# Optimization experiments

Hardware: AMD Instinct MI355X
Metric: run time of the kernel (lower is better)

Reference implementation:

```python
import jax, jax.numpy as jnp
import numpy as np

N_NODES = 4096
N_EDGES = 65536
BS = 16
LEAKY_SLOPE = 0.01
BN_EPS = 1e-5


def _init(key, shape, scale=0.02):
    return (jax.random.normal(key, shape, dtype=jnp.float32) * scale)


def setup_inputs() -> dict:
    key = jax.random.key(0)
    ks = jax.random.split(key, 20)
    x_in = jax.random.normal(ks[0], (N_NODES, 8500), dtype=jnp.float32)
    edge_index = jax.random.randint(ks[1], (2, N_EDGES), 0, N_NODES, dtype=jnp.int64)
    return {
        "x_in": x_in,
        "edge_index": edge_index,
        # SAGEConv params: Wl (neighbor lin, with bias), Wr (root lin, no bias)
        "W1l": _init(ks[2], (320, 8500)), "b1": jnp.zeros((320,), jnp.float32), "W1r": _init(ks[3], (320, 8500)),
        "W2l": _init(ks[4], (180, 320)),  "b2": jnp.zeros((180,), jnp.float32), "W2r": _init(ks[5], (180, 320)),
        "W3l": _init(ks[6], (90, 180)),   "b3": jnp.zeros((90,), jnp.float32),  "W3r": _init(ks[7], (90, 180)),
        "W4l": _init(ks[8], (50, 90)),    "b4": jnp.zeros((50,), jnp.float32),  "W4r": _init(ks[9], (50, 90)),
        "Wf1": _init(ks[10], (32, 50)),   "bf1": jnp.zeros((32,), jnp.float32),
        "Wf2": _init(ks[11], (16, 32)),   "bf2": jnp.zeros((16,), jnp.float32),
        "Wf3": _init(ks[12], (1, 16)),    "bf3": jnp.zeros((1,), jnp.float32),
    }


def _sage(x, src, dst, Wl, bl, Wr):
    # PyG SAGEConv: out = lin_l(mean_{j in N(i)} x_j) + lin_r(x_i)
    agg = jax.ops.segment_sum(x[src], dst, num_segments=N_NODES)          # [N, F]
    deg = jax.ops.segment_sum(jnp.ones_like(dst, dtype=x.dtype), dst, num_segments=N_NODES)
    mean = agg / jnp.maximum(deg, 1.0)[:, None]
    return mean @ Wl.T + bl + x @ Wr.T


def _leaky(x):
    return jnp.where(x >= 0, x, LEAKY_SLOPE * x)


def _bn(x):
    # F.batch_norm(x, None, None, training=True): per-feature, biased var, no affine
    m = jnp.mean(x, axis=0)
    v = jnp.mean((x - m) ** 2, axis=0)
    return (x - m) / jnp.sqrt(v + BN_EPS)


def reference(x_in, edge_index,
              W1l, b1, W1r, W2l, b2, W2r, W3l, b3, W3r, W4l, b4, W4r,
              Wf1, bf1, Wf2, bf2, Wf3, bf3):
    src, dst = edge_index[0], edge_index[1]
    x = _bn(_leaky(_sage(x_in, src, dst, W1l, b1, W1r)))
    x = _bn(_leaky(_sage(x, src, dst, W2l, b2, W2r)))
    x = _bn(_leaky(_sage(x, src, dst, W3l, b3, W3r)))
    x = _bn(_leaky(_sage(x, src, dst, W4l, b4, W4r)))
    # get_batch: label i -> floor(i / (N/BS)); global_add_pool == segment sum
    x = x.reshape(BS, N_NODES // BS, -1).sum(axis=1)                      # [BS, 50]
    x = x @ Wf1.T + bf1
    x = x @ Wf2.T + bf2
    x = x @ Wf3.T + bf3
    return x
```

## Files before the change

kernel.cpp:

```cpp
#include <hip/hip_runtime.h>
#include <stdint.h>

#define NN 4096
#define NE 65536
#define LEAKY 0.01f
#define BN_EPS 1e-5f
#define DSTRIDE 96

typedef float f32x4 __attribute__((ext_vector_type(4)));
typedef __bf16 bf16x8 __attribute__((ext_vector_type(8)));
typedef unsigned short u16x8 __attribute__((ext_vector_type(8)));

static __device__ __forceinline__ unsigned short f2bf(float v) {
  unsigned int u = __float_as_uint(v);
  u += 0x7fff + ((u >> 16) & 1);
  return (unsigned short)(u >> 16);
}

typedef __attribute__((address_space(1))) void gvoid;
typedef __attribute__((address_space(3))) void lvoid;

static __device__ __forceinline__ void async16(const void* g, void* l) {
  __builtin_amdgcn_global_load_lds((gvoid*)(uintptr_t)g,
                                   (lvoid*)(uint32_t)(uintptr_t)l, 16, 0, 0);
}


static __device__ __forceinline__ void pack_w_seg(int lblk, const float* __restrict__ Wl,
                                                  const float* __restrict__ Wr,
                                                  unsigned short* __restrict__ dst,
                                                  int Fout, int Fin, int Kp, int Np) {
  int nb = Kp >> 3;
  int idx = lblk * 256 + threadIdx.x;
  if (idx >= Np * nb) return;
  int row = idx / nb, kb = idx - row * nb;
  int g = kb >> 3, b = kb & 7;
  int dkb = (g << 3) | ((b + row) & 7);
  const float* src = nullptr;
  if (row < Fout)          src = Wl + (size_t)row * Fin;
  else if (row < 2 * Fout) src = Wr + (size_t)(row - Fout) * Fin;
  u16x8 st;
#pragma unroll
  for (int o = 0; o < 8; ++o) {
    int k = kb * 8 + o;
    float v = (src && k < Fin) ? src[k] : 0.f;
    st[o] = f2bf(v);
  }
  *(u16x8*)&dst[(size_t)row * Kp + dkb * 8] = st;
}

#define ADJ_BLK    256
#define PW1_BLK   2660
#define PW2_BLK     60
#define PW3_BLK     24
#define PW4_BLK      8
#define SETUP_BLK (ADJ_BLK + PW1_BLK + PW2_BLK + PW3_BLK + PW4_BLK)

__global__ __launch_bounds__(256) void setup_all(
    const int* __restrict__ esrc, const int* __restrict__ edst,
    const float* __restrict__ W1l, const float* __restrict__ W1r,
    const float* __restrict__ W2l, const float* __restrict__ W2r,
    const float* __restrict__ W3l, const float* __restrict__ W3r,
    const float* __restrict__ W4l, const float* __restrict__ W4r,
    unsigned short* __restrict__ wb1, unsigned short* __restrict__ wb2,
    unsigned short* __restrict__ wb3, unsigned short* __restrict__ wb4,
    int* __restrict__ deg, int* __restrict__ eix) {
  int blk = blockIdx.x;
  if (blk < ADJ_BLK) {
    int e = blk * 256 + threadIdx.x;
    int d = edst[e];
    int pos = atomicAdd(&deg[d], 1);
    if (pos < DSTRIDE) eix[(size_t)d * DSTRIDE + pos] = esrc[e];
  } else if (blk < ADJ_BLK + PW1_BLK) {
    pack_w_seg(blk - ADJ_BLK, W1l, W1r, wb1, 320, 8500, 8512, 640);
  } else if (blk < ADJ_BLK + PW1_BLK + PW2_BLK) {
    pack_w_seg(blk - ADJ_BLK - PW1_BLK, W2l, W2r, wb2, 180, 320, 320, 384);
  } else if (blk < ADJ_BLK + PW1_BLK + PW2_BLK + PW3_BLK) {
    pack_w_seg(blk - ADJ_BLK - PW1_BLK - PW2_BLK, W3l, W3r, wb3, 90, 180, 192, 256);
  } else {
    pack_w_seg(blk - ADJ_BLK - PW1_BLK - PW2_BLK - PW3_BLK, W4l, W4r, wb4,
               50, 90, 128, 128);
  }
}

__global__ __launch_bounds__(256) void gemm_f32a(const float* __restrict__ X,
                                                 const unsigned short* __restrict__ B,
                                                 float* __restrict__ C, int N, int M) {
  const int K = 8512, KS = 133, FIN = 8500;
  __shared__ unsigned short smem[3 * 128 * 64];
  unsigned short* As = smem;

  const int t = threadIdx.x;
  const int bm = blockIdx.x, bn = blockIdx.y;
  const int lane = t & 63;
  const int wave = t >> 6;
  const int wm = (wave & 1) * 64, wn = (wave >> 1) * 64;
  const int l16 = lane & 15, quad = lane >> 4;

  const int gz = (int)gridDim.z, z = (int)blockIdx.z;
  const int per = KS / gz, rem = KS % gz;
  const int k0 = z * per + (z < rem ? z : rem);
  const int k1 = k0 + per + (z < rem ? 1 : 0);

  f32x4 acc[4][4];
#pragma unroll
  for (int i = 0; i < 4; ++i)
#pragma unroll
    for (int j = 0; j < 4; ++j) acc[i][j] = (f32x4){0.f, 0.f, 0.f, 0.f};

  const int srow = t >> 3;
  const int bblk = t & 7;
  const int scol = bblk * 8;
  const float* Xb = X + (size_t)(bm * 128) * FIN;
  const unsigned short* Bbase = B + (size_t)(bn * 128) * K + scol;

  float va[4][8];
  auto loadA = [&](int kt) {
    int gc = kt * 64 + scol;
#pragma unroll
    for (int p = 0; p < 4; ++p) {
      const float* ap = Xb + (size_t)(p * 32 + srow) * FIN + gc;
      if (gc + 8 <= FIN) {
        f32x4 a = *(const f32x4*)ap;
        f32x4 b2 = *(const f32x4*)(ap + 4);
#pragma unroll
        for (int o = 0; o < 4; ++o) { va[p][o] = a[o]; va[p][o + 4] = b2[o]; }
      } else {
#pragma unroll
        for (int o = 0; o < 8; ++o) va[p][o] = (gc + o < FIN) ? ap[o] : 0.f;
      }
    }
  };
  auto writeA = [&]() {
#pragma unroll
    for (int p = 0; p < 4; ++p) {
      int row = p * 32 + srow;
      int rot = ((bblk + row) & 7) * 8;
      bf16x8 bv;
#pragma unroll
      for (int o = 0; o < 8; ++o) bv[o] = (__bf16)va[p][o];
      *(bf16x8*)&As[row * 64 + rot] = bv;
    }
  };
  auto stageB = [&](int kt, int bb) {
    unsigned short* Bd = smem + 128 * 64 + bb * 128 * 64;
#pragma unroll
    for (int p = 0; p < 4; ++p) {
      int row = p * 32 + srow;
      async16(Bbase + (size_t)row * K + kt * 64, &Bd[row * 64 + scol]);
    }
  };

  loadA(k0);
  stageB(k0, 0);
  writeA();
  __syncthreads();

  int bb = 0;
  for (int kt = k0; kt < k1; ++kt) {
    bool more = (kt + 1 < k1);
    if (more) {
      loadA(kt + 1);
      stageB(kt + 1, bb ^ 1);
    }
    const unsigned short* Bs = smem + 128 * 64 + bb * 128 * 64;
#pragma unroll
    for (int kh = 0; kh < 2; ++kh) {
      const int s8 = ((kh * 4 + quad + l16) & 7) * 8;
      bf16x8 af[4], bfr[4];
#pragma unroll
      for (int i = 0; i < 4; ++i)
        af[i] = *(const bf16x8*)&As[(wm + i * 16 + l16) * 64 + s8];
#pragma unroll
      for (int j = 0; j < 4; ++j)
        bfr[j] = *(const bf16x8*)&Bs[(wn + j * 16 + l16) * 64 + s8];
#pragma unroll
      for (int i = 0; i < 4; ++i)
#pragma unroll
        for (int j = 0; j < 4; ++j)
          acc[i][j] = __builtin_amdgcn_mfma_f32_16x16x32_bf16(af[i], bfr[j], acc[i][j], 0, 0, 0);
    }
    __syncthreads();
    if (more) {
      writeA();
      __syncthreads();
      bb ^= 1;
    }
  }

  float* Cb = C + (size_t)blockIdx.z * M * N;
#pragma unroll
  for (int i = 0; i < 4; ++i) {
    int rbase = bm * 128 + wm + i * 16 + quad * 4;
#pragma unroll
    for (int j = 0; j < 4; ++j) {
      int col = bn * 128 + wn + j * 16 + l16;
      float* cp = Cb + (size_t)rbase * N + col;
#pragma unroll
      for (int r = 0; r < 4; ++r) cp[(size_t)r * N] = acc[i][j][r];
    }
  }
}

__global__ __launch_bounds__(256) void gemm_bt(const unsigned short* __restrict__ A,
                                               const unsigned short* __restrict__ B,
                                               float* __restrict__ C, int N, int K,
                                               int M) {
  __shared__ unsigned short smem[2 * 128 * 64];
  unsigned short* As = smem;
  unsigned short* Bs = smem + 128 * 64;

  const int t = threadIdx.x;
  const int bm = blockIdx.x, bn = blockIdx.y;
  const int lane = t & 63;
  const int wave = t >> 6;
  const int wm = (wave & 1) * 64, wn = (wave >> 1) * 64;
  const int l16 = lane & 15, quad = lane >> 4;

  const int ksteps = K >> 6;

  f32x4 acc[4][4];
#pragma unroll
  for (int i = 0; i < 4; ++i)
#pragma unroll
    for (int j = 0; j < 4; ++j) acc[i][j] = (f32x4){0.f, 0.f, 0.f, 0.f};

  const int srow = t >> 3;
  const int scol = (t & 7) * 8;
  const unsigned short* Abase = A + (size_t)(bm * 128) * K + scol;
  const unsigned short* Bbase = B + (size_t)(bn * 128) * K + scol;

  for (int kt = 0; kt < ksteps; ++kt) {
    const unsigned short* Ag = Abase + kt * 64;
    const unsigned short* Bg = Bbase + kt * 64;
#pragma unroll
    for (int p = 0; p < 4; ++p) {
      int row = p * 32 + srow;
      async16(Ag + (size_t)row * K, &As[row * 64 + scol]);
    }
#pragma unroll
    for (int p = 0; p < 4; ++p) {
      int row = p * 32 + srow;
      async16(Bg + (size_t)row * K, &Bs[row * 64 + scol]);
    }
    __syncthreads();
#pragma unroll
    for (int kh = 0; kh < 2; ++kh) {
      const int s8 = ((kh * 4 + quad + l16) & 7) * 8;
      bf16x8 af[4], bfr[4];
#pragma unroll
      for (int i = 0; i < 4; ++i)
        af[i] = *(const bf16x8*)&As[(wm + i * 16 + l16) * 64 + s8];
#pragma unroll
      for (int j = 0; j < 4; ++j)
        bfr[j] = *(const bf16x8*)&Bs[(wn + j * 16 + l16) * 64 + s8];
#pragma unroll
      for (int i = 0; i < 4; ++i)
#pragma unroll
        for (int j = 0; j < 4; ++j)
          acc[i][j] = __builtin_amdgcn_mfma_f32_16x16x32_bf16(af[i], bfr[j], acc[i][j], 0, 0, 0);
    }
    __syncthreads();
  }

#pragma unroll
  for (int i = 0; i < 4; ++i) {
    int rbase = bm * 128 + wm + i * 16 + quad * 4;
#pragma unroll
    for (int j = 0; j < 4; ++j) {
      int col = bn * 128 + wn + j * 16 + l16;
      float* cp = C + (size_t)rbase * N + col;
#pragma unroll
      for (int r = 0; r < 4; ++r) cp[(size_t)r * N] = acc[i][j][r];
    }
  }
}

__global__ void reduceN(float* __restrict__ y, int nz) {
  int idx = blockIdx.x * 256 + threadIdx.x;
  f32x4* p = (f32x4*)y;
  const int S = NN * 640 / 4;
  f32x4 v = p[idx];
  for (int sl = 1; sl < nz; ++sl) v += p[idx + (size_t)sl * S];
  p[idx] = v;
}

__global__ __launch_bounds__(256) void sage_agg(
    const float* __restrict__ y, const int* __restrict__ deg,
    const int* __restrict__ eix, const float* __restrict__ bias,
    float* __restrict__ z, int F, int ldy) {
  int i = blockIdx.x;
  int tx = threadIdx.x, ty = threadIdx.y;
  __shared__ int se[DSTRIDE];
  __shared__ float red[3][64][4];
  int d = deg[i]; if (d > DSTRIDE) d = DSTRIDE;
  {
    int lt = ty * 64 + tx;
    if (lt < d) se[lt] = eix[(size_t)i * DSTRIDE + lt];
  }
  __syncthreads();
  int nfb = (F + 255) >> 8;
  for (int fb = 0; fb < nfb; ++fb) {
    int f4 = (fb * 64 + tx) * 4;
    bool active = (f4 < F);
    f32x4 s = {0.f, 0.f, 0.f, 0.f};
    if (active) {
      const float* yb = y + f4;
      int e = ty;
      for (; e + 4 < d; e += 8) {
        f32x4 a = *(const f32x4*)&yb[(size_t)se[e] * ldy];
        f32x4 b = *(const f32x4*)&yb[(size_t)se[e + 4] * ldy];
        s += a; s += b;
      }
      if (e < d) s += *(const f32x4*)&yb[(size_t)se[e] * ldy];
    }
    if (ty > 0) *(f32x4*)red[ty - 1][tx] = s;
    __syncthreads();
    if (ty == 0 && active) {
      s += *(const f32x4*)red[0][tx];
      s += *(const f32x4*)red[1][tx];
      s += *(const f32x4*)red[2][tx];
      float inv = 1.f / (float)(d > 1 ? d : 1);
      int cnt = F - f4; if (cnt > 4) cnt = 4;
      const float* yr = &y[(size_t)i * ldy + F + f4];
      float* zo = &z[(size_t)i * F + f4];
      for (int j = 0; j < cnt; ++j) {
        float w = s[j] * inv + yr[j] + bias[f4 + j];
        zo[j] = (w >= 0.f) ? w : LEAKY * w;
      }
    }
    if (fb + 1 < nfb) __syncthreads();
  }
}


__global__ __launch_bounds__(256) void bn_part(const float* __restrict__ z,
                                               float* __restrict__ sums, int F) {
  int tx = threadIdx.x, ty = threadIdx.y;
  int f = blockIdx.x * 64 + tx;
  float s = 0.f, s2 = 0.f;
  if (f < F) {
    int r0 = blockIdx.y * 512 + ty * 128;
    for (int j = 0; j < 128; ++j) {
      float v = z[(size_t)(r0 + j) * F + f];
      s += v; s2 += v * v;
    }
  }
  __shared__ float ls[4][64], ls2[4][64];
  ls[ty][tx] = s; ls2[ty][tx] = s2;
  __syncthreads();
  if (ty == 0 && f < F) {
    float S  = ls[0][tx] + ls[1][tx] + ls[2][tx] + ls[3][tx];
    float S2 = ls2[0][tx] + ls2[1][tx] + ls2[2][tx] + ls2[3][tx];
    atomicAdd(&sums[f], S);
    atomicAdd(&sums[F + f], S2);
  }
}

__global__ void bn_norm8(const float* __restrict__ z, const float* __restrict__ sums,
                         unsigned short* __restrict__ xout, int F, int Kp) {
  int nb = Kp >> 3;
  int idx = blockIdx.x * 256 + threadIdx.x;
  int row = idx / nb, kb = idx - row * nb;
  int g = kb >> 3, b = kb & 7;
  int dkb = (g << 3) | ((b + row) & 7);
  u16x8 st;
#pragma unroll
  for (int o = 0; o < 8; ++o) {
    int k = kb * 8 + o;
    float v = 0.f;
    if (k < F) {
      float m  = sums[k] * (1.f / NN);
      float var = sums[F + k] * (1.f / NN) - m * m;
      float rs = rsqrtf(var + BN_EPS);
      v = (z[(size_t)row * F + k] - m) * rs;
    }
    st[o] = f2bf(v);
  }
  *(u16x8*)&xout[(size_t)row * Kp + dkb * 8] = st;
}

__global__ void pool_fc(const float* __restrict__ z,
                        const float* __restrict__ sums,
                        const float* __restrict__ Wf1, const float* __restrict__ bf1,
                        const float* __restrict__ Wf2, const float* __restrict__ bf2,
                        const float* __restrict__ Wf3, const float* __restrict__ bf3,
                        float* __restrict__ out) {
  __shared__ float pool[50];
  __shared__ float h1[32], h2[16];
  int b = blockIdx.x, t = threadIdx.x;
  if (t < 50) {
    float s = 0.f;
    for (int r = 0; r < 256; ++r) s += z[(size_t)(b * 256 + r) * 50 + t];
    float m  = sums[t] * (1.f / NN);
    float var = sums[50 + t] * (1.f / NN) - m * m;
    float rs = rsqrtf(var + BN_EPS);
    pool[t] = (s - 256.f * m) * rs;
  }
  __syncthreads();
  if (t < 32) {
    float s = bf1[t];
    for (int f = 0; f < 50; ++f) s += pool[f] * Wf1[t * 50 + f];
    h1[t] = s;
  }
  __syncthreads();
  if (t < 16) {
    float s = bf2[t];
    for (int f = 0; f < 32; ++f) s += h1[f] * Wf2[t * 32 + f];
    h2[t] = s;
  }
  __syncthreads();
  if (t == 0) {
    float s = bf3[0];
    for (int f = 0; f < 16; ++f) s += h2[f] * Wf3[f];
    out[b] = s;
  }
}


extern "C" void kernel_launch(void* const* d_in, const int* in_sizes, int n_in,
                              void* d_out, int out_size, void* d_ws, size_t ws_size,
                              hipStream_t stream) {
  const float* x_in = (const float*)d_in[0];
  const int* ei = (const int*)d_in[1];
  const float* W1l = (const float*)d_in[2];
  const float* b1  = (const float*)d_in[3];
  const float* W1r = (const float*)d_in[4];
  const float* W2l = (const float*)d_in[5];
  const float* b2  = (const float*)d_in[6];
  const float* W2r = (const float*)d_in[7];
  const float* W3l = (const float*)d_in[8];
  const float* b3  = (const float*)d_in[9];
  const float* W3r = (const float*)d_in[10];
  const float* W4l = (const float*)d_in[11];
  const float* b4  = (const float*)d_in[12];
  const float* W4r = (const float*)d_in[13];
  const float* Wf1 = (const float*)d_in[14];
  const float* bf1 = (const float*)d_in[15];
  const float* Wf2 = (const float*)d_in[16];
  const float* bf2 = (const float*)d_in[17];
  const float* Wf3 = (const float*)d_in[18];
  const float* bf3 = (const float*)d_in[19];
  float* out = (float*)d_out;
  (void)in_sizes; (void)n_in; (void)out_size;

  char* ws = (char*)d_ws;
  size_t off = 0;
  auto alloc = [&](size_t bytes) -> void* {
    void* p = ws + off;
    off = (off + bytes + 255) & ~(size_t)255;
    return p;
  };
  unsigned short* xbf = (unsigned short*)alloc((size_t)NN * 320 * 2);
  unsigned short* wb1 = (unsigned short*)alloc((size_t)640 * 8512 * 2);
  unsigned short* wb2 = (unsigned short*)alloc((size_t)384 * 320 * 2);
  unsigned short* wb3 = (unsigned short*)alloc((size_t)256 * 192 * 2);
  unsigned short* wb4 = (unsigned short*)alloc((size_t)128 * 128 * 2);
  float* z    = (float*)alloc((size_t)NN * 320 * 4);
  int* deg    = (int*)alloc(NN * 4);
  float* bnsum = (float*)alloc(1280 * 4);
  int* eix    = (int*)alloc((size_t)NN * DSTRIDE * 4);
  const size_t YS = (size_t)NN * 640 * 4;
  float* y = (float*)(ws + off);
  const int nz = 4;
  if (off + (size_t)nz * YS > ws_size) return;
  float* bns1 = bnsum;
  float* bns2 = bnsum + 640;
  float* bns3 = bnsum + 1000;
  float* bns4 = bnsum + 1180;

  hipMemsetAsync(deg, 0, NN * 4 + 1280 * 4, stream);

  setup_all<<<dim3(SETUP_BLK), dim3(256), 0, stream>>>(
      ei, ei + NE, W1l, W1r, W2l, W2r, W3l, W3r, W4l, W4r,
      wb1, wb2, wb3, wb4, deg, eix);

  gemm_f32a<<<dim3(32, 5, nz), dim3(256), 0, stream>>>(x_in, wb1, y, 640, NN);
  reduceN<<<dim3(NN * 640 / 4 / 256), dim3(256), 0, stream>>>(y, nz);
  sage_agg<<<dim3(NN), dim3(64, 4), 0, stream>>>(y, deg, eix, b1, z, 320, 640);
  bn_part<<<dim3(5, 8), dim3(64, 4), 0, stream>>>(z, bns1, 320);
  bn_norm8<<<dim3(NN * 40 / 256), dim3(256), 0, stream>>>(z, bns1, xbf, 320, 320);

  gemm_bt<<<dim3(32, 3, 1), dim3(256), 0, stream>>>(xbf, wb2, y, 384, 320, NN);
  sage_agg<<<dim3(NN), dim3(64, 4), 0, stream>>>(y, deg, eix, b2, z, 180, 384);
  bn_part<<<dim3(3, 8), dim3(64, 4), 0, stream>>>(z, bns2, 180);
  bn_norm8<<<dim3(NN * 24 / 256), dim3(256), 0, stream>>>(z, bns2, xbf, 180, 192);

  gemm_bt<<<dim3(32, 2, 1), dim3(256), 0, stream>>>(xbf, wb3, y, 256, 192, NN);
  sage_agg<<<dim3(NN), dim3(64, 4), 0, stream>>>(y, deg, eix, b3, z, 90, 256);
  bn_part<<<dim3(2, 8), dim3(64, 4), 0, stream>>>(z, bns3, 90);
  bn_norm8<<<dim3(NN * 16 / 256), dim3(256), 0, stream>>>(z, bns3, xbf, 90, 128);

  gemm_bt<<<dim3(32, 1, 1), dim3(256), 0, stream>>>(xbf, wb4, y, 128, 128, NN);
  sage_agg<<<dim3(NN), dim3(64, 4), 0, stream>>>(y, deg, eix, b4, z, 50, 128);
  bn_part<<<dim3(1, 8), dim3(64, 4), 0, stream>>>(z, bns4, 50);

  pool_fc<<<dim3(16), dim3(64), 0, stream>>>(z, bns4, Wf1, bf1, Wf2, bf2, Wf3, bf3, out);
}
```

Before: 486.0 us.

## Double-buffer A tile and deepen gemm_f32a pipeline with manual waitcnt barriers

Restructures the main layer-1 GEMM loop so the bf16-converted A tile is double-buffered in LDS alongside B. The fp32 global loads for A are issued two stages ahead into alternating register sets. The two __syncthreads per iteration become one hand-written s_waitcnt/s_barrier that leaves 8 vector loads in flight, and sched_barrier fences pin the instruction order. This targets load latency and barrier stalls, at the cost of more LDS (64KB), more registers, and fragile manual waitcnt counts.

```diff
diff --git a/kernel.cpp b/kernel.cpp
--- a/kernel.cpp
+++ b/kernel.cpp
@@ -24,6 +24,10 @@
   __builtin_amdgcn_global_load_lds((gvoid*)(uintptr_t)g,
                                    (lvoid*)(uint32_t)(uintptr_t)l, 16, 0, 0);
 }
+
+#define SCHED_FENCE() __builtin_amdgcn_sched_barrier(0)
+#define WAITBAR8() asm volatile("s_waitcnt lgkmcnt(0)\n\ts_waitcnt vmcnt(8)\n\ts_barrier" ::: "memory")
+#define WAITBAR0() asm volatile("s_waitcnt lgkmcnt(0)\n\ts_waitcnt vmcnt(0)\n\ts_barrier" ::: "memory")
 
 
 static __device__ __forceinline__ void pack_w_seg(int lblk, const float* __restrict__ Wl,
@@ -87,8 +91,8 @@
                                                  const unsigned short* __restrict__ B,
                                                  float* __restrict__ C, int N, int M) {
   const int K = 8512, KS = 133, FIN = 8500;
-  __shared__ unsigned short smem[3 * 128 * 64];
-  unsigned short* As = smem;
+  __shared__ unsigned short As0[128 * 64], As1[128 * 64];
+  __shared__ unsigned short Bs0[128 * 64], Bs1[128 * 64];
 
   const int t = threadIdx.x;
   const int bm = blockIdx.x, bn = blockIdx.y;
@@ -114,8 +118,9 @@
   const float* Xb = X + (size_t)(bm * 128) * FIN;
   const unsigned short* Bbase = B + (size_t)(bn * 128) * K + scol;
 
-  float va[4][8];
-  auto loadA = [&](int kt) {
+  float vaA[4][8], vaB[4][8];
+
+  auto loadA = [&](int kt, float (&va)[4][8]) {
     int gc = kt * 64 + scol;
 #pragma unroll
     for (int p = 0; p < 4; ++p) {
@@ -131,7 +136,7 @@
       }
     }
   };
-  auto writeA = [&]() {
+  auto writeA = [&](unsigned short* As, float (&va)[4][8]) {
 #pragma unroll
     for (int p = 0; p < 4; ++p) {
       int row = p * 32 + srow;
@@ -142,28 +147,14 @@
       *(bf16x8*)&As[row * 64 + rot] = bv;
     }
   };
-  auto stageB = [&](int kt, int bb) {
-    unsigned short* Bd = smem + 128 * 64 + bb * 128 * 64;
+  auto stageB = [&](int kt, unsigned short* Bd) {
 #pragma unroll
     for (int p = 0; p < 4; ++p) {
       int row = p * 32 + srow;
       async16(Bbase + (size_t)row * K + kt * 64, &Bd[row * 64 + scol]);
     }
   };
-
-  loadA(k0);
-  stageB(k0, 0);
-  writeA();
-  __syncthreads();
-
-  int bb = 0;
-  for (int kt = k0; kt < k1; ++kt) {
-    bool more = (kt + 1 < k1);
-    if (more) {
-      loadA(kt + 1);
-      stageB(kt + 1, bb ^ 1);
-    }
-    const unsigned short* Bs = smem + 128 * 64 + bb * 128 * 64;
+  auto mfma_step = [&](const unsigned short* As, const unsigned short* Bs) {
 #pragma unroll
     for (int kh = 0; kh < 2; ++kh) {
       const int s8 = ((kh * 4 + quad + l16) & 7) * 8;
@@ -180,12 +171,46 @@
         for (int j = 0; j < 4; ++j)
           acc[i][j] = __builtin_amdgcn_mfma_f32_16x16x32_bf16(af[i], bfr[j], acc[i][j], 0, 0, 0);
     }
-    __syncthreads();
-    if (more) {
-      writeA();
-      __syncthreads();
-      bb ^= 1;
-    }
+  };
+
+  loadA(k0, vaA);
+  SCHED_FENCE();
+  stageB(k0, Bs0);
+  SCHED_FENCE();
+  writeA(As0, vaA);
+  SCHED_FENCE();
+  bool pm = (k0 + 1 < k1);
+  if (pm) loadA(k0 + 1, vaA);
+  SCHED_FENCE();
+  if (pm) WAITBAR8(); else WAITBAR0();
+
+  int kt = k0;
+  for (;;) {
+    {
+      bool s = kt + 1 < k1, l = kt + 2 < k1;
+      if (s) stageB(kt + 1, Bs1);
+      SCHED_FENCE();
+      if (l) loadA(kt + 2, vaB);
+      SCHED_FENCE();
+      if (s) writeA(As1, vaA);
+      SCHED_FENCE();
+      mfma_step(As0, Bs0);
+      if (!s) break;
+      if (l) WAITBAR8(); else WAITBAR0();
+    }
+    {
+      bool s = kt + 2 < k1, l = kt + 3 < k1;
+      if (s) stageB(kt + 2, Bs0);
+      SCHED_FENCE();
+      if (l) loadA(kt + 3, vaA);
+      SCHED_FENCE();
+      if (s) writeA(As0, vaB);
+      SCHED_FENCE();
+      mfma_step(As1, Bs1);
+      if (!s) break;
+      if (l) WAITBAR8(); else WAITBAR0();
+    }
+    kt += 2;
   }
 
   float* Cb = C + (size_t)blockIdx.z * M * N;
```

Result: slower. 594.5 us (+22.3%).

## Stage fp32 A tiles via async LDS loads and reduce split-K with atomics

Applied to the files above, without the earlier changes.

The first-layer GEMM now streams fp32 X tiles directly into LDS with global_load_lds, using a rotated layout and a zero-pad source for the K tail, and converts them to bf16 when building MFMA fragments. The old register-staged convert-and-store path and the B double buffering are both removed. Split-K rises from 4 to 8 slices, and the separate reduceN pass is replaced by atomic adds into a zeroed output. This is meant to cut register pressure and VGPR round trips, and to remove an extra kernel and its partial-sum traffic. In exchange it loses load/compute overlap within each block, adds contended fp32 atomics, and makes the summation order nondeterministic.

```diff
diff --git a/kernel.cpp b/kernel.cpp
--- a/kernel.cpp
+++ b/kernel.cpp
@@ -85,10 +85,12 @@
 
 __global__ __launch_bounds__(256) void gemm_f32a(const float* __restrict__ X,
                                                  const unsigned short* __restrict__ B,
-                                                 float* __restrict__ C, int N, int M) {
+                                                 float* __restrict__ C,
+                                                 const float* __restrict__ zpad,
+                                                 int N, int M) {
   const int K = 8512, KS = 133, FIN = 8500;
-  __shared__ unsigned short smem[3 * 128 * 64];
-  unsigned short* As = smem;
+  __shared__ float As32[128 * 64];
+  __shared__ unsigned short Bs[128 * 64];
 
   const int t = threadIdx.x;
   const int bm = blockIdx.x, bn = blockIdx.y;
@@ -108,69 +110,54 @@
 #pragma unroll
     for (int j = 0; j < 4; ++j) acc[i][j] = (f32x4){0.f, 0.f, 0.f, 0.f};
 
+  int rowA[8], logA[8];
+  const float* gA[8];
+#pragma unroll
+  for (int j = 0; j < 8; ++j) {
+    int row = wave * 32 + j * 4 + (lane >> 4);
+    int phys = lane & 15;
+    int lg = (phys - row) & 15;
+    rowA[j] = row; logA[j] = lg;
+    gA[j] = X + (size_t)(bm * 128 + row) * FIN + lg * 4;
+  }
   const int srow = t >> 3;
-  const int bblk = t & 7;
-  const int scol = bblk * 8;
-  const float* Xb = X + (size_t)(bm * 128) * FIN;
+  const int scol = (t & 7) * 8;
   const unsigned short* Bbase = B + (size_t)(bn * 128) * K + scol;
 
-  float va[4][8];
-  auto loadA = [&](int kt) {
-    int gc = kt * 64 + scol;
-#pragma unroll
-    for (int p = 0; p < 4; ++p) {
-      const float* ap = Xb + (size_t)(p * 32 + srow) * FIN + gc;
-      if (gc + 8 <= FIN) {
-        f32x4 a = *(const f32x4*)ap;
-        f32x4 b2 = *(const f32x4*)(ap + 4);
-#pragma unroll
-        for (int o = 0; o < 4; ++o) { va[p][o] = a[o]; va[p][o + 4] = b2[o]; }
-      } else {
-#pragma unroll
-        for (int o = 0; o < 8; ++o) va[p][o] = (gc + o < FIN) ? ap[o] : 0.f;
+  for (int kt = k0; kt < k1; ++kt) {
+    if (kt < 132) {
+#pragma unroll
+      for (int j = 0; j < 8; ++j)
+        async16(gA[j] + (size_t)kt * 64, &As32[rowA[j] * 64 + (lane & 15) * 4]);
+    } else {
+#pragma unroll
+      for (int j = 0; j < 8; ++j) {
+        const float* s = (kt * 64 + logA[j] * 4 < FIN) ? gA[j] + (size_t)kt * 64 : zpad;
+        async16(s, &As32[rowA[j] * 64 + (lane & 15) * 4]);
       }
     }
-  };
-  auto writeA = [&]() {
 #pragma unroll
     for (int p = 0; p < 4; ++p) {
       int row = p * 32 + srow;
-      int rot = ((bblk + row) & 7) * 8;
-      bf16x8 bv;
-#pragma unroll
-      for (int o = 0; o < 8; ++o) bv[o] = (__bf16)va[p][o];
-      *(bf16x8*)&As[row * 64 + rot] = bv;
-    }
-  };
-  auto stageB = [&](int kt, int bb) {
-    unsigned short* Bd = smem + 128 * 64 + bb * 128 * 64;
-#pragma unroll
-    for (int p = 0; p < 4; ++p) {
-      int row = p * 32 + srow;
-      async16(Bbase + (size_t)row * K + kt * 64, &Bd[row * 64 + scol]);
-    }
-  };
-
-  loadA(k0);
-  stageB(k0, 0);
-  writeA();
-  __syncthreads();
-
-  int bb = 0;
-  for (int kt = k0; kt < k1; ++kt) {
-    bool more = (kt + 1 < k1);
-    if (more) {
-      loadA(kt + 1);
-      stageB(kt + 1, bb ^ 1);
-    }
-    const unsigned short* Bs = smem + 128 * 64 + bb * 128 * 64;
+      async16(Bbase + (size_t)row * K + kt * 64, &Bs[row * 64 + scol]);
+    }
+    __syncthreads();
 #pragma unroll
     for (int kh = 0; kh < 2; ++kh) {
+      const int q2 = (kh * 4 + quad) * 2;
       const int s8 = ((kh * 4 + quad + l16) & 7) * 8;
       bf16x8 af[4], bfr[4];
 #pragma unroll
-      for (int i = 0; i < 4; ++i)
-        af[i] = *(const bf16x8*)&As[(wm + i * 16 + l16) * 64 + s8];
+      for (int i = 0; i < 4; ++i) {
+        int row = wm + i * 16 + l16;
+        f32x4 a0 = *(const f32x4*)&As32[row * 64 + ((q2 + row) & 15) * 4];
+        f32x4 a1 = *(const f32x4*)&As32[row * 64 + ((q2 + 1 + row) & 15) * 4];
+#pragma unroll
+        for (int o = 0; o < 4; ++o) {
+          af[i][o] = (__bf16)a0[o];
+          af[i][o + 4] = (__bf16)a1[o];
+        }
+      }
 #pragma unroll
       for (int j = 0; j < 4; ++j)
         bfr[j] = *(const bf16x8*)&Bs[(wn + j * 16 + l16) * 64 + s8];
@@ -181,23 +168,17 @@
           acc[i][j] = __builtin_amdgcn_mfma_f32_16x16x32_bf16(af[i], bfr[j], acc[i][j], 0, 0, 0);
     }
     __syncthreads();
-    if (more) {
-      writeA();
-      __syncthreads();
-      bb ^= 1;
-    }
-  }
-
-  float* Cb = C + (size_t)blockIdx.z * M * N;
+  }
+
 #pragma unroll
   for (int i = 0; i < 4; ++i) {
     int rbase = bm * 128 + wm + i * 16 + quad * 4;
 #pragma unroll
     for (int j = 0; j < 4; ++j) {
       int col = bn * 128 + wn + j * 16 + l16;
-      float* cp = Cb + (size_t)rbase * N + col;
-#pragma unroll
-      for (int r = 0; r < 4; ++r) cp[(size_t)r * N] = acc[i][j][r];
+      float* cp = C + (size_t)rbase * N + col;
+#pragma unroll
+      for (int r = 0; r < 4; ++r) unsafeAtomicAdd(&cp[(size_t)r * N], acc[i][j][r]);
     }
   }
 }
@@ -274,15 +255,6 @@
       for (int r = 0; r < 4; ++r) cp[(size_t)r * N] = acc[i][j][r];
     }
   }
-}
-
-__global__ void reduceN(float* __restrict__ y, int nz) {
-  int idx = blockIdx.x * 256 + threadIdx.x;
-  f32x4* p = (f32x4*)y;
-  const int S = NN * 640 / 4;
-  f32x4 v = p[idx];
-  for (int sl = 1; sl < nz; ++sl) v += p[idx + (size_t)sl * S];
-  p[idx] = v;
 }
 
 __global__ __launch_bounds__(256) void sage_agg(
@@ -459,24 +431,24 @@
   float* z    = (float*)alloc((size_t)NN * 320 * 4);
   int* deg    = (int*)alloc(NN * 4);
   float* bnsum = (float*)alloc(1280 * 4);
+  float* zpad  = (float*)alloc(256);
   int* eix    = (int*)alloc((size_t)NN * DSTRIDE * 4);
   const size_t YS = (size_t)NN * 640 * 4;
   float* y = (float*)(ws + off);
-  const int nz = 4;
-  if (off + (size_t)nz * YS > ws_size) return;
+  if (off + YS > ws_size) return;
   float* bns1 = bnsum;
   float* bns2 = bnsum + 640;
   float* bns3 = bnsum + 1000;
   float* bns4 = bnsum + 1180;
 
-  hipMemsetAsync(deg, 0, NN * 4 + 1280 * 4, stream);
+  hipMemsetAsync(deg, 0, NN * 4 + 1280 * 4 + 256, stream);
+  hipMemsetAsync(y, 0, YS, stream);
 
   setup_all<<<dim3(SETUP_BLK), dim3(256), 0, stream>>>(
       ei, ei + NE, W1l, W1r, W2l, W2r, W3l, W3r, W4l, W4r,
       wb1, wb2, wb3, wb4, deg, eix);
 
-  gemm_f32a<<<dim3(32, 5, nz), dim3(256), 0, stream>>>(x_in, wb1, y, 640, NN);
-  reduceN<<<dim3(NN * 640 / 4 / 256), dim3(256), 0, stream>>>(y, nz);
+  gemm_f32a<<<dim3(32, 5, 8), dim3(256), 0, stream>>>(x_in, wb1, y, zpad, 640, NN);
   sage_agg<<<dim3(NN), dim3(64, 4), 0, stream>>>(y, deg, eix, b1, z, 320, 640);
   bn_part<<<dim3(5, 8), dim3(64, 4), 0, stream>>>(z, bns1, 320);
   bn_norm8<<<dim3(NN * 40 / 256), dim3(256), 0, stream>>>(z, bns1, xbf, 320, 320);
```

Result: slower. 503.6 us (+3.6%).

## Load A fragments directly into registers and raise split-K to 8 slices

Applied to the files above, without the earlier changes.

The layer-1 GEMM no longer stages the fp32 input tile through shared memory. Each wave loads its A rows straight from global memory into registers in MFMA fragment layout, converts them to bf16 there, and keeps only B double-buffered in LDS, which removes one barrier and the LDS writes and reads for A per k-step. Split-K goes from 4 to 8 slices when the workspace allows, to put more blocks in flight. In exchange, A is loaded redundantly by the two waves that share rows, the loads are less coalesced, register pressure rises, and the reduction pass has more partial buffers to sum.

```diff
diff --git a/kernel.cpp b/kernel.cpp
--- a/kernel.cpp
+++ b/kernel.cpp
@@ -83,12 +83,11 @@
   }
 }
 
-__global__ __launch_bounds__(256) void gemm_f32a(const float* __restrict__ X,
+__global__ __launch_bounds__(256) void gemm_areg(const float* __restrict__ X,
                                                  const unsigned short* __restrict__ B,
                                                  float* __restrict__ C, int N, int M) {
   const int K = 8512, KS = 133, FIN = 8500;
-  __shared__ unsigned short smem[3 * 128 * 64];
-  unsigned short* As = smem;
+  __shared__ unsigned short Bs[2][128 * 64];
 
   const int t = threadIdx.x;
   const int bm = blockIdx.x, bn = blockIdx.y;
@@ -108,42 +107,59 @@
 #pragma unroll
     for (int j = 0; j < 4; ++j) acc[i][j] = (f32x4){0.f, 0.f, 0.f, 0.f};
 
+  const float* Arow[4];
+#pragma unroll
+  for (int i = 0; i < 4; ++i)
+    Arow[i] = X + (size_t)(bm * 128 + wm + i * 16 + l16) * FIN + quad * 8;
+
+  f32x4 pf[4][2][2];
+  bf16x8 curA[4][2];
+
+  auto loadA = [&](int kt) {
+    if (kt < 132) {
+#pragma unroll
+      for (int i = 0; i < 4; ++i) {
+        const float* p = Arow[i] + (size_t)kt * 64;
+        pf[i][0][0] = *(const f32x4*)p;
+        pf[i][0][1] = *(const f32x4*)(p + 4);
+        pf[i][1][0] = *(const f32x4*)(p + 32);
+        pf[i][1][1] = *(const f32x4*)(p + 36);
+      }
+    } else {
+#pragma unroll
+      for (int i = 0; i < 4; ++i)
+#pragma unroll
+        for (int kh = 0; kh < 2; ++kh)
+#pragma unroll
+          for (int h = 0; h < 2; ++h) {
+            f32x4 v = (f32x4){0.f, 0.f, 0.f, 0.f};
+            int cb = kt * 64 + kh * 32 + quad * 8 + h * 4;
+#pragma unroll
+            for (int o = 0; o < 4; ++o)
+              if (cb + o < FIN) v[o] = Arow[i][(size_t)kt * 64 + kh * 32 + h * 4 + o];
+            pf[i][kh][h] = v;
+          }
+    }
+  };
+  auto cvtA = [&]() {
+#pragma unroll
+    for (int i = 0; i < 4; ++i)
+#pragma unroll
+      for (int kh = 0; kh < 2; ++kh) {
+        bf16x8 c;
+#pragma unroll
+        for (int o = 0; o < 4; ++o) {
+          c[o]     = (__bf16)pf[i][kh][0][o];
+          c[o + 4] = (__bf16)pf[i][kh][1][o];
+        }
+        curA[i][kh] = c;
+      }
+  };
   const int srow = t >> 3;
-  const int bblk = t & 7;
-  const int scol = bblk * 8;
-  const float* Xb = X + (size_t)(bm * 128) * FIN;
+  const int scol = (t & 7) * 8;
   const unsigned short* Bbase = B + (size_t)(bn * 128) * K + scol;
-
-  float va[4][8];
-  auto loadA = [&](int kt) {
-    int gc = kt * 64 + scol;
-#pragma unroll
-    for (int p = 0; p < 4; ++p) {
-      const float* ap = Xb + (size_t)(p * 32 + srow) * FIN + gc;
-      if (gc + 8 <= FIN) {
-        f32x4 a = *(const f32x4*)ap;
-        f32x4 b2 = *(const f32x4*)(ap + 4);
-#pragma unroll
-        for (int o = 0; o < 4; ++o) { va[p][o] = a[o]; va[p][o + 4] = b2[o]; }
-      } else {
-#pragma unroll
-        for (int o = 0; o < 8; ++o) va[p][o] = (gc + o < FIN) ? ap[o] : 0.f;
-      }
-    }
-  };
-  auto writeA = [&]() {
-#pragma unroll
-    for (int p = 0; p < 4; ++p) {
-      int row = p * 32 + srow;
-      int rot = ((bblk + row) & 7) * 8;
-      bf16x8 bv;
-#pragma unroll
-      for (int o = 0; o < 8; ++o) bv[o] = (__bf16)va[p][o];
-      *(bf16x8*)&As[row * 64 + rot] = bv;
-    }
-  };
   auto stageB = [&](int kt, int bb) {
-    unsigned short* Bd = smem + 128 * 64 + bb * 128 * 64;
+    unsigned short* Bd = Bs[bb];
 #pragma unroll
     for (int p = 0; p < 4; ++p) {
       int row = p * 32 + srow;
@@ -153,8 +169,8 @@
 
   loadA(k0);
   stageB(k0, 0);
-  writeA();
   __syncthreads();
+  cvtA();
 
   int bb = 0;
   for (int kt = k0; kt < k1; ++kt) {
@@ -163,27 +179,22 @@
       loadA(kt + 1);
       stageB(kt + 1, bb ^ 1);
     }
-    const unsigned short* Bs = smem + 128 * 64 + bb * 128 * 64;
 #pragma unroll
     for (int kh = 0; kh < 2; ++kh) {
       const int s8 = ((kh * 4 + quad + l16) & 7) * 8;
-      bf16x8 af[4], bfr[4];
+      bf16x8 bfr[4];
+#pragma unroll
+      for (int j = 0; j < 4; ++j)
+        bfr[j] = *(const bf16x8*)&Bs[bb][(wn + j * 16 + l16) * 64 + s8];
 #pragma unroll
       for (int i = 0; i < 4; ++i)
-        af[i] = *(const bf16x8*)&As[(wm + i * 16 + l16) * 64 + s8];
-#pragma unroll
-      for (int j = 0; j < 4; ++j)
-        bfr[j] = *(const bf16x8*)&Bs[(wn + j * 16 + l16) * 64 + s8];
-#pragma unroll
-      for (int i = 0; i < 4; ++i)
 #pragma unroll
         for (int j = 0; j < 4; ++j)
-          acc[i][j] = __builtin_amdgcn_mfma_f32_16x16x32_bf16(af[i], bfr[j], acc[i][j], 0, 0, 0);
-    }
-    __syncthreads();
+          acc[i][j] = __builtin_amdgcn_mfma_f32_16x16x32_bf16(curA[i][kh], bfr[j], acc[i][j], 0, 0, 0);
+    }
     if (more) {
-      writeA();
       __syncthreads();
+      cvtA();
       bb ^= 1;
     }
   }
@@ -462,7 +473,7 @@
   int* eix    = (int*)alloc((size_t)NN * DSTRIDE * 4);
   const size_t YS = (size_t)NN * 640 * 4;
   float* y = (float*)(ws + off);
-  const int nz = 4;
+  int nz = (off + 8 * YS <= ws_size) ? 8 : 4;
   if (off + (size_t)nz * YS > ws_size) return;
   float* bns1 = bnsum;
   float* bns2 = bnsum + 640;
@@ -475,7 +486,7 @@
       ei, ei + NE, W1l, W1r, W2l, W2r, W3l, W3r, W4l, W4r,
       wb1, wb2, wb3, wb4, deg, eix);
 
-  gemm_f32a<<<dim3(32, 5, nz), dim3(256), 0, stream>>>(x_in, wb1, y, 640, NN);
+  gemm_areg<<<dim3(32, 5, nz), dim3(256), 0, stream>>>(x_in, wb1, y, 640, NN);
   reduceN<<<dim3(NN * 640 / 4 / 256), dim3(256), 0, stream>>>(y, nz);
   sage_agg<<<dim3(NN), dim3(64, 4), 0, stream>>>(y, deg, eix, b1, z, 320, 640);
   bn_part<<<dim3(5, 8), dim3(64, 4), 0, stream>>>(z, bns1, 320);
```

Result: slower. 537.9 us (+10.7%).
